# Performance work log

Measured on AMD Instinct MI355X. Metric: run time of the kernel, lower is better.

The kernel has to match this reference:

```python
import jax, jax.numpy as jnp
import numpy as np

B, CIN, COUT, H, W = 16, 64, 64, 256, 256
M1, M2 = 32, 32


def setup_inputs() -> dict:
    key = jax.random.key(0)
    k = jax.random.split(key, 7)
    x = jax.random.normal(k[0], (B, CIN, H, W), dtype=jnp.float32)
    # emulate int8 quantized weights: stored values in [-128, 127]
    q_weights1 = jax.random.randint(k[1], (CIN, COUT, M1, M2, 2), -128, 128, dtype=jnp.int32)
    q_weights2 = jax.random.randint(k[2], (CIN, COUT, M1, M2, 2), -128, 128, dtype=jnp.int32)
    w1_scale = jax.random.uniform(k[3], (1,), dtype=jnp.float32) * 0.01 + 0.001
    w1_min = jax.random.normal(k[4], (1,), dtype=jnp.float32) * 0.1
    w2_scale = jax.random.uniform(k[5], (1,), dtype=jnp.float32) * 0.01 + 0.001
    w2_min = jax.random.normal(k[6], (1,), dtype=jnp.float32) * 0.1
    return {"x": x, "q_weights1": q_weights1, "q_weights2": q_weights2,
            "w1_scale": w1_scale, "w1_min": w1_min,
            "w2_scale": w2_scale, "w2_min": w2_min}


def _dequant_complex(q, scale, min_val):
    # (q + 127) * scale + min, then view last dim (re, im) as complex
    w = (q.astype(jnp.float32) + 127.0) * scale + min_val
    return jax.lax.complex(w[..., 0], w[..., 1])


def reference(x, q_weights1, q_weights2, w1_scale, w1_min, w2_scale, w2_min):
    b, cin, h, w = x.shape
    # rfft2 with ortho norm, complex64
    x_ft = jnp.fft.rfft2(x, norm="ortho")  # [B, Cin, H, W//2+1]

    w1c = _dequant_complex(q_weights1, w1_scale[0], w1_min[0])  # [Cin, Cout, M1, M2]
    w2c = _dequant_complex(q_weights2, w2_scale[0], w2_min[0])

    # complex multiply + channel contraction on the retained low/high modes
    out1 = jnp.einsum("bixy,ioxy->boxy", x_ft[:, :, :M1, :M2], w1c)
    out2 = jnp.einsum("bixy,ioxy->boxy", x_ft[:, :, h - M1:, :M2], w2c)

    out_ft = jnp.zeros((b, COUT, h, w // 2 + 1), dtype=x_ft.dtype)
    out_ft = out_ft.at[:, :, :M1, :M2].set(out1)
    out_ft = out_ft.at[:, :, h - M1:, :M2].set(out2)

    return jnp.fft.irfft2(out_ft, s=(h, w), norm="ortho")  # [B, Cout, H, W] float32
```

## Files before the change

### kernel.cpp

```cpp
#include <hip/hip_runtime.h>
#include <math.h>

#define NB 16
#define NCIN 64
#define NCOUT 64
#define NH 256
#define NW 256
#define NM 64
#define NKX 32
#define INV256 (1.0f/256.0f)

typedef __attribute__((ext_vector_type(8))) short short8v;
typedef __attribute__((ext_vector_type(4))) float f32x4;
typedef unsigned short u16;
typedef unsigned int u32;

__device__ __forceinline__ void bf16_split(float v, u16& hi, u16& lo) {
    u32 b = __float_as_uint(v);
    u32 hib = b & 0xffff0000u;
    float lof = v - __uint_as_float(hib);
    hi = (u16)(hib >> 16);
    lo = (u16)(__float_as_uint(lof) >> 16);
}

__device__ __forceinline__ u16 bf16_rtn(float v) {
    u32 b = __float_as_uint(v);
    u32 r = b + 0x7fffu + ((b >> 16) & 1u);
    return (u16)(r >> 16);
}

__global__ __launch_bounds__(256) void init_tw(u16* __restrict__ tw) {
    const int tid = blockIdx.x * 256 + threadIdx.x;
    const float TWO_PI = 6.28318530717958647692f;
    if (tid < 16384) {
        const int e = tid & 7, lane = (tid >> 3) & 63;
        const int nt = (tid >> 9) & 3, kc = tid >> 11;
        const int w = kc * 32 + (lane >> 4) * 8 + e;
        const int n = nt * 16 + (lane & 15);
        const int kx = n >> 1, p = n & 1;
        const float ang = TWO_PI * (float)((kx * w) & 255) * INV256;
        const float v = p ? -sinf(ang) : cosf(ang);
        u16 hi, lo; bf16_split(v, hi, lo);
        tw[tid] = hi; tw[16384 + tid] = lo;
    } else {
        const int u = tid - 16384;
        const int e = u & 7, lane = (u >> 3) & 63;
        const int kc = (u >> 9) & 7, mt = u >> 12;
        const int m = mt * 16 + (lane & 15);
        const int h = kc * 32 + (lane >> 4) * 8 + e;
        const int ky = (m < 32) ? m : (192 + m);
        const float ang = TWO_PI * (float)((ky * h) & 255) * INV256;
        const float c = cosf(ang), s = sinf(ang);
        u16 hi, lo;
        bf16_split(c,  hi, lo); tw[32768 + u] = hi; tw[49152 + u]  = lo;
        bf16_split(s,  hi, lo); tw[65536 + u] = hi; tw[81920 + u]  = lo;
        bf16_split(-s, hi, lo); tw[98304 + u] = hi; tw[114688 + u] = lo;
    }
}

__global__ __launch_bounds__(256) void init_tw2(u16* __restrict__ tw2) {
    const int tid = blockIdx.x * 256 + threadIdx.x;
    const float TWO_PI = 6.28318530717958647692f;
    if (tid < 16384) {
        const int e = tid & 7, lane = (tid >> 3) & 63;
        const int kc = (tid >> 9) & 1, HT = tid >> 10;
        const int h = HT * 16 + (lane & 15);
        const int m = kc * 32 + ((lane >> 4) << 3) + e;
        const int ky = (m < 32) ? m : (192 + m);
        const float ang = TWO_PI * (float)((ky * h) & 255) * INV256;
        tw2[tid]         = bf16_rtn(cosf(ang));
        tw2[16384 + tid] = bf16_rtn(sinf(ang));
        tw2[32768 + tid] = bf16_rtn(-sinf(ang));
    } else {
        const int u = tid - 16384;
        const int e = u & 7, lane = (u >> 3) & 63;
        const int kc = (u >> 9) & 1, nt = u >> 10;
        const int w = nt * 16 + (lane & 15);
        const int kk = kc * 32 + ((lane >> 4) << 3) + e;
        const int kx = kk >> 1, c = kk & 1;
        const float wt = (kx == 0) ? 1.f : 2.f;
        const float ang = TWO_PI * (float)((kx * w) & 255) * INV256;
        const float v = c ? (-wt * sinf(ang) * INV256) : (wt * cosf(ang) * INV256);
        tw2[49152 + u] = bf16_rtn(v);
    }
}

__global__ __launch_bounds__(256) void fwd_mfma(const float* __restrict__ x,
                                                const u16* __restrict__ tw,
                                                float2* __restrict__ xft) {
    __shared__ u16 planes[4 * 32 * 264];
    const int t = threadIdx.x;
    const int lane = t & 63;
    const int wv = t >> 6;
    const int l15 = lane & 15;
    const int lk = lane >> 4;
    const float* __restrict__ xb = x + (size_t)blockIdx.x * (NH * NW);

    const u16* __restrict__ T1h = tw;
    const u16* __restrict__ T1l = tw + 16384;

    for (int mt = 0; mt < 4; ++mt) {
        const int hbase = wv * 64 + mt * 16;
        f32x4 acc[4] = {f32x4{0,0,0,0}, f32x4{0,0,0,0}, f32x4{0,0,0,0}, f32x4{0,0,0,0}};
        for (int kc = 0; kc < 8; ++kc) {
            const float* xr = xb + (size_t)(hbase + l15) * NW + kc * 32 + lk * 8;
            const float4 xa = *(const float4*)xr;
            const float4 xc = *(const float4*)(xr + 4);
            const float v[8] = {xa.x, xa.y, xa.z, xa.w, xc.x, xc.y, xc.z, xc.w};
            short8v Ah, Al;
            #pragma unroll
            for (int e = 0; e < 8; ++e) {
                u16 hi, lo; bf16_split(v[e], hi, lo);
                Ah[e] = (short)hi; Al[e] = (short)lo;
            }
            const int tbase = (kc * 4) * 512 + lane * 8;
            #pragma unroll
            for (int nt = 0; nt < 4; ++nt) {
                const short8v Bh = *(const short8v*)(T1h + tbase + nt * 512);
                const short8v Bl = *(const short8v*)(T1l + tbase + nt * 512);
                acc[nt] = __builtin_amdgcn_mfma_f32_16x16x32_bf16(Ah, Bh, acc[nt], 0, 0, 0);
                acc[nt] = __builtin_amdgcn_mfma_f32_16x16x32_bf16(Ah, Bl, acc[nt], 0, 0, 0);
                acc[nt] = __builtin_amdgcn_mfma_f32_16x16x32_bf16(Al, Bh, acc[nt], 0, 0, 0);
            }
        }
        #pragma unroll
        for (int nt = 0; nt < 4; ++nt) {
            const int n = nt * 16 + l15;
            const int kx = n >> 1, p = n & 1;
            #pragma unroll
            for (int r = 0; r < 4; ++r) {
                const int h = hbase + lk * 4 + r;
                u16 hi, lo; bf16_split(acc[nt][r], hi, lo);
                planes[(2 * p) * 8448 + kx * 264 + h] = hi;
                planes[(2 * p + 1) * 8448 + kx * 264 + h] = lo;
            }
        }
    }
    __syncthreads();

    const u16* __restrict__ C2h = tw + 32768;
    const u16* __restrict__ C2l = tw + 49152;
    const u16* __restrict__ S2h = tw + 65536;
    const u16* __restrict__ S2l = tw + 81920;
    const u16* __restrict__ Snh = tw + 98304;
    const u16* __restrict__ Snl = tw + 114688;

    f32x4 zre[2] = {f32x4{0,0,0,0}, f32x4{0,0,0,0}};
    f32x4 zim[2] = {f32x4{0,0,0,0}, f32x4{0,0,0,0}};
    for (int kc = 0; kc < 8; ++kc) {
        const int abase = (wv * 8 + kc) * 512 + lane * 8;
        const short8v Ch = *(const short8v*)(C2h + abase);
        const short8v Cl = *(const short8v*)(C2l + abase);
        const short8v Sh = *(const short8v*)(S2h + abase);
        const short8v Sl = *(const short8v*)(S2l + abase);
        const short8v Nh = *(const short8v*)(Snh + abase);
        const short8v Nl = *(const short8v*)(Snl + abase);
        #pragma unroll
        for (int nt = 0; nt < 2; ++nt) {
            const int kx = nt * 16 + l15;
            const int off = kx * 264 + kc * 32 + lk * 8;
            const short8v Yrh = *(const short8v*)(planes + off);
            const short8v Yrl = *(const short8v*)(planes + 8448 + off);
            const short8v Yih = *(const short8v*)(planes + 16896 + off);
            const short8v Yil = *(const short8v*)(planes + 25344 + off);
            zre[nt] = __builtin_amdgcn_mfma_f32_16x16x32_bf16(Ch, Yrh, zre[nt], 0, 0, 0);
            zre[nt] = __builtin_amdgcn_mfma_f32_16x16x32_bf16(Ch, Yrl, zre[nt], 0, 0, 0);
            zre[nt] = __builtin_amdgcn_mfma_f32_16x16x32_bf16(Cl, Yrh, zre[nt], 0, 0, 0);
            zre[nt] = __builtin_amdgcn_mfma_f32_16x16x32_bf16(Sh, Yih, zre[nt], 0, 0, 0);
            zre[nt] = __builtin_amdgcn_mfma_f32_16x16x32_bf16(Sh, Yil, zre[nt], 0, 0, 0);
            zre[nt] = __builtin_amdgcn_mfma_f32_16x16x32_bf16(Sl, Yih, zre[nt], 0, 0, 0);
            zim[nt] = __builtin_amdgcn_mfma_f32_16x16x32_bf16(Ch, Yih, zim[nt], 0, 0, 0);
            zim[nt] = __builtin_amdgcn_mfma_f32_16x16x32_bf16(Ch, Yil, zim[nt], 0, 0, 0);
            zim[nt] = __builtin_amdgcn_mfma_f32_16x16x32_bf16(Cl, Yih, zim[nt], 0, 0, 0);
            zim[nt] = __builtin_amdgcn_mfma_f32_16x16x32_bf16(Nh, Yrh, zim[nt], 0, 0, 0);
            zim[nt] = __builtin_amdgcn_mfma_f32_16x16x32_bf16(Nh, Yrl, zim[nt], 0, 0, 0);
            zim[nt] = __builtin_amdgcn_mfma_f32_16x16x32_bf16(Nl, Yrh, zim[nt], 0, 0, 0);
        }
    }
    float2* __restrict__ op = xft + (size_t)blockIdx.x * (NM * NKX);
    #pragma unroll
    for (int nt = 0; nt < 2; ++nt) {
        const int kx = nt * 16 + l15;
        #pragma unroll
        for (int r = 0; r < 4; ++r) {
            const int m = wv * 16 + lk * 4 + r;
            op[m * NKX + kx] = make_float2(zre[nt][r] * INV256, zim[nt][r] * INV256);
        }
    }
}

__global__ __launch_bounds__(256) void mode_v8(const float2* __restrict__ xft,
                                               const int* __restrict__ q1,
                                               const int* __restrict__ q2,
                                               const float* __restrict__ w1s,
                                               const float* __restrict__ w1m,
                                               const float* __restrict__ w2s,
                                               const float* __restrict__ w2m,
                                               float2* __restrict__ oft) {
    __shared__ float2 xs[2][8][16][8];
    __shared__ float2 ws[2][8][16][10];
    const int m  = blockIdx.x;
    const int og = blockIdx.y;
    const int kh = blockIdx.z;
    const int t = threadIdx.x;
    const int b = t >> 4, o = t & 15;
    const int mm = (m < 32) ? m : (m - 32);
    const int* __restrict__ q = (m < 32) ? q1 : q2;
    const float scale = (m < 32) ? w1s[0] : w2s[0];
    const float wmin  = (m < 32) ? w1m[0] : w2m[0];

    const int row = t >> 1;
    const int il = row >> 4, rb = row & 15, half = t & 1;

    const float4* __restrict__ xf4 = (const float4*)xft;
    const int4*   __restrict__ qi4 = (const int4*)q;
    const size_t xbase = (size_t)(rb * 64 + il) * 1024 + m * 16 + kh * 4 + half * 2;
    const size_t wbase = (size_t)(il * 64 + og * 16 + rb) * 512 + mm * 16 + kh * 4 + half * 2;

    float4 px0, px1; int4 pw0, pw1;

    #define MV8_LOAD(P)                                                        \
        px0 = xf4[xbase + (size_t)(P) * 8 * 1024];                             \
        px1 = xf4[xbase + (size_t)(P) * 8 * 1024 + 1];                         \
        pw0 = qi4[wbase + (size_t)(P) * 8 * 32768];                            \
        pw1 = qi4[wbase + (size_t)(P) * 8 * 32768 + 1];

    #define MV8_WRITE(BUF)                                                     \
        {                                                                      \
            float4* xd = (float4*)&xs[BUF][il][rb][half * 4];                  \
            xd[0] = px0; xd[1] = px1;                                          \
            float4* wd = (float4*)&ws[BUF][il][rb][half * 4];                  \
            wd[0] = make_float4(((float)pw0.x + 127.f) * scale + wmin,         \
                                ((float)pw0.y + 127.f) * scale + wmin,         \
                                ((float)pw0.z + 127.f) * scale + wmin,         \
                                ((float)pw0.w + 127.f) * scale + wmin);        \
            wd[1] = make_float4(((float)pw1.x + 127.f) * scale + wmin,         \
                                ((float)pw1.y + 127.f) * scale + wmin,         \
                                ((float)pw1.z + 127.f) * scale + wmin,         \
                                ((float)pw1.w + 127.f) * scale + wmin);        \
        }

    MV8_LOAD(0)
    MV8_WRITE(0)
    __syncthreads();

    float accr[8], acci[8];
    #pragma unroll
    for (int k = 0; k < 8; ++k) { accr[k] = 0.f; acci[k] = 0.f; }

    #pragma unroll 1
    for (int p = 0; p < 8; ++p) {
        const int cur = p & 1;
        if (p < 7) { MV8_LOAD(p + 1) }
        #pragma unroll
        for (int jl = 0; jl < 8; ++jl) {
            const float4* xr4 = (const float4*)&xs[cur][jl][b][0];
            const float4* wr4 = (const float4*)&ws[cur][jl][o][0];
            #pragma unroll
            for (int kq = 0; kq < 4; ++kq) {
                const float4 xv = xr4[kq];
                const float4 wv = wr4[kq];
                accr[2 * kq]     += xv.x * wv.x - xv.y * wv.y;
                acci[2 * kq]     += xv.x * wv.y + xv.y * wv.x;
                accr[2 * kq + 1] += xv.z * wv.z - xv.w * wv.w;
                acci[2 * kq + 1] += xv.z * wv.w + xv.w * wv.z;
            }
        }
        if (p < 7) {
            MV8_WRITE(cur ^ 1)
            __syncthreads();
        }
    }
    #undef MV8_LOAD
    #undef MV8_WRITE

    float2* __restrict__ op = oft + ((size_t)(b * 64 + og * 16 + o) * NM + m) * NKX + kh * 8;
    #pragma unroll
    for (int k = 0; k < 8; ++k) op[k] = make_float2(accr[k], acci[k]);
}

__global__ __launch_bounds__(256) void inv_mfma(const float2* __restrict__ oft,
                                                const u16* __restrict__ tw2,
                                                float* __restrict__ out) {
    __shared__ u16 lds[13824];
    const int t = threadIdx.x;
    const int lane = t & 63;
    const int wv = t >> 6;
    const int l15 = lane & 15;
    const int lk = lane >> 4;
    const int hh = blockIdx.y;

    const float2* __restrict__ ip = oft + (size_t)blockIdx.x * (NM * NKX);
    #pragma unroll
    for (int r = 0; r < 8; ++r) {
        const int idx = r * 256 + t;
        const int m = idx >> 5, kx = idx & 31;
        const float2 v = ip[idx];
        lds[kx * 72 + m]        = bf16_rtn(v.x);
        lds[2304 + kx * 72 + m] = bf16_rtn(v.y);
    }
    __syncthreads();

    const u16* __restrict__ C4 = tw2;
    const u16* __restrict__ S4 = tw2 + 16384;
    const u16* __restrict__ N4 = tw2 + 32768;

    short8v Br[2][2], Bi[2][2];
    #pragma unroll
    for (int nt = 0; nt < 2; ++nt) {
        #pragma unroll
        for (int kc = 0; kc < 2; ++kc) {
            const int off = (nt * 16 + l15) * 72 + kc * 32 + lk * 8;
            Br[nt][kc] = *(const short8v*)(lds + off);
            Bi[nt][kc] = *(const short8v*)(lds + 2304 + off);
        }
    }

    #pragma unroll
    for (int mt = 0; mt < 2; ++mt) {
        const int lt = wv * 2 + mt;
        const int HT = hh * 8 + lt;
        f32x4 zr[2] = {f32x4{0,0,0,0}, f32x4{0,0,0,0}};
        f32x4 zi[2] = {f32x4{0,0,0,0}, f32x4{0,0,0,0}};
        #pragma unroll
        for (int kc = 0; kc < 2; ++kc) {
            const int abase = ((HT * 2 + kc) * 64 + lane) * 8;
            const short8v C = *(const short8v*)(C4 + abase);
            const short8v S = *(const short8v*)(S4 + abase);
            const short8v N = *(const short8v*)(N4 + abase);
            #pragma unroll
            for (int nt = 0; nt < 2; ++nt) {
                zr[nt] = __builtin_amdgcn_mfma_f32_16x16x32_bf16(C, Br[nt][kc], zr[nt], 0, 0, 0);
                zr[nt] = __builtin_amdgcn_mfma_f32_16x16x32_bf16(N, Bi[nt][kc], zr[nt], 0, 0, 0);
                zi[nt] = __builtin_amdgcn_mfma_f32_16x16x32_bf16(S, Br[nt][kc], zi[nt], 0, 0, 0);
                zi[nt] = __builtin_amdgcn_mfma_f32_16x16x32_bf16(C, Bi[nt][kc], zi[nt], 0, 0, 0);
            }
        }
        #pragma unroll
        for (int nt = 0; nt < 2; ++nt) {
            const int kx = nt * 16 + l15;
            #pragma unroll
            for (int r = 0; r < 4; ++r) {
                const int hl = lt * 16 + lk * 4 + r;
                const u32 pk = (u32)bf16_rtn(zr[nt][r]) | ((u32)bf16_rtn(zi[nt][r]) << 16);
                *(u32*)(lds + 4608 + hl * 72 + 2 * kx) = pk;
            }
        }
    }
    __syncthreads();

    const u16* __restrict__ W5 = tw2 + 49152;
    float* __restrict__ op = out + (size_t)blockIdx.x * (NH * NW) + (size_t)hh * 128 * NW;
    for (int nt = 0; nt < 16; ++nt) {
        const short8v B0 = *(const short8v*)(W5 + ((nt * 2 + 0) * 64 + lane) * 8);
        const short8v B1 = *(const short8v*)(W5 + ((nt * 2 + 1) * 64 + lane) * 8);
        const int w = nt * 16 + l15;
        #pragma unroll
        for (int mt = 0; mt < 2; ++mt) {
            const int lt = wv * 2 + mt;
            const int h0 = lt * 16 + l15;
            const short8v A0 = *(const short8v*)(lds + 4608 + h0 * 72 + lk * 8);
            const short8v A1 = *(const short8v*)(lds + 4608 + h0 * 72 + 32 + lk * 8);
            f32x4 acc = {0, 0, 0, 0};
            acc = __builtin_amdgcn_mfma_f32_16x16x32_bf16(A0, B0, acc, 0, 0, 0);
            acc = __builtin_amdgcn_mfma_f32_16x16x32_bf16(A1, B1, acc, 0, 0, 0);
            #pragma unroll
            for (int r = 0; r < 4; ++r) {
                const int hl = lt * 16 + lk * 4 + r;
                op[hl * 256 + w] = acc[r];
            }
        }
    }
}

extern "C" void kernel_launch(void* const* d_in, const int* in_sizes, int n_in,
                              void* d_out, int out_size, void* d_ws, size_t ws_size,
                              hipStream_t stream) {
    const float* x  = (const float*)d_in[0];
    const int* q1   = (const int*)d_in[1];
    const int* q2   = (const int*)d_in[2];
    const float* w1s = (const float*)d_in[3];
    const float* w1m = (const float*)d_in[4];
    const float* w2s = (const float*)d_in[5];
    const float* w2m = (const float*)d_in[6];
    float* out = (float*)d_out;

    float2* xft = (float2*)d_ws;
    float2* oft = xft + (size_t)NB * NCIN * NM * NKX;
    u16* tw  = (u16*)((char*)d_ws + (size_t)48 * 1024 * 1024);
    u16* tw2 = tw + 131072;

    init_tw<<<128, 256, 0, stream>>>(tw);
    init_tw2<<<128, 256, 0, stream>>>(tw2);
    fwd_mfma<<<NB * NCIN, 256, 0, stream>>>(x, tw, xft);
    mode_v8<<<dim3(NM, 4, 4), 256, 0, stream>>>(xft, q1, q2, w1s, w1m, w2s, w2m, oft);
    inv_mfma<<<dim3(NB * NCOUT, 2), 256, 0, stream>>>(oft, tw2, out);
}
```

Before: 240.8 us.

## Restructure mode-mixing kernel: stage all weights once, stream x directly from global

The mode-mixing kernel is rewritten to use a finer grid (8 output-channel groups × 8 kx groups) so each block handles 8 output channels and 4 kx values. Each block dequantizes its full weight tile for all 64 input channels into LDS once, behind a single barrier. It then streams x directly from global memory with 8-deep register prefetch instead of double-buffered LDS staging with per-step barriers. This removes repeated synchronization and raises block count and parallelism. In exchange, per-thread register reuse drops (2 outputs per thread instead of 8) and x is read from global redundantly across output-channel groups.

```diff
diff --git a/kernel.cpp b/kernel.cpp
--- a/kernel.cpp
+++ b/kernel.cpp
@@ -189,94 +189,80 @@
     }
 }
 
-__global__ __launch_bounds__(256) void mode_v8(const float2* __restrict__ xft,
-                                               const int* __restrict__ q1,
-                                               const int* __restrict__ q2,
-                                               const float* __restrict__ w1s,
-                                               const float* __restrict__ w1m,
-                                               const float* __restrict__ w2s,
-                                               const float* __restrict__ w2m,
-                                               float2* __restrict__ oft) {
-    __shared__ float2 xs[2][8][16][8];
-    __shared__ float2 ws[2][8][16][10];
+__global__ __launch_bounds__(256) void mode_v10(const float2* __restrict__ xft,
+                                                const int* __restrict__ q1,
+                                                const int* __restrict__ q2,
+                                                const float* __restrict__ w1s,
+                                                const float* __restrict__ w1m,
+                                                const float* __restrict__ w2s,
+                                                const float* __restrict__ w2m,
+                                                float2* __restrict__ oft) {
+    __shared__ float wlds[4096];
     const int m  = blockIdx.x;
     const int og = blockIdx.y;
     const int kh = blockIdx.z;
     const int t = threadIdx.x;
-    const int b = t >> 4, o = t & 15;
     const int mm = (m < 32) ? m : (m - 32);
     const int* __restrict__ q = (m < 32) ? q1 : q2;
     const float scale = (m < 32) ? w1s[0] : w2s[0];
     const float wmin  = (m < 32) ? w1m[0] : w2m[0];
 
-    const int row = t >> 1;
-    const int il = row >> 4, rb = row & 15, half = t & 1;
-
+    {
+        const int4* __restrict__ qi4 = (const int4*)q;
+        int4 v[4];
+        #pragma unroll
+        for (int rr = 0; rr < 2; ++rr) {
+            const int row = t * 2 + rr;
+            const int i = row >> 3, ol = row & 7;
+            const size_t b4 = (size_t)(i * 64 + og * 8 + ol) * 512 + mm * 16 + kh * 2;
+            v[rr * 2]     = qi4[b4];
+            v[rr * 2 + 1] = qi4[b4 + 1];
+        }
+        #pragma unroll
+        for (int rr = 0; rr < 2; ++rr) {
+            const int row = t * 2 + rr;
+            float* wd = &wlds[row * 8];
+            const int4 a = v[rr * 2], bq = v[rr * 2 + 1];
+            wd[0] = ((float)a.x + 127.f) * scale + wmin;
+            wd[1] = ((float)a.y + 127.f) * scale + wmin;
+            wd[2] = ((float)a.z + 127.f) * scale + wmin;
+            wd[3] = ((float)a.w + 127.f) * scale + wmin;
+            wd[4] = ((float)bq.x + 127.f) * scale + wmin;
+            wd[5] = ((float)bq.y + 127.f) * scale + wmin;
+            wd[6] = ((float)bq.z + 127.f) * scale + wmin;
+            wd[7] = ((float)bq.w + 127.f) * scale + wmin;
+        }
+    }
+    __syncthreads();
+
+    const int b  = t >> 4;
+    const int ol = (t >> 1) & 7;
+    const int kp = t & 1;
     const float4* __restrict__ xf4 = (const float4*)xft;
-    const int4*   __restrict__ qi4 = (const int4*)q;
-    const size_t xbase = (size_t)(rb * 64 + il) * 1024 + m * 16 + kh * 4 + half * 2;
-    const size_t wbase = (size_t)(il * 64 + og * 16 + rb) * 512 + mm * 16 + kh * 4 + half * 2;
-
-    float4 px0, px1; int4 pw0, pw1;
-
-    #define MV8_LOAD(P)                                                        \
-        px0 = xf4[xbase + (size_t)(P) * 8 * 1024];                             \
-        px1 = xf4[xbase + (size_t)(P) * 8 * 1024 + 1];                         \
-        pw0 = qi4[wbase + (size_t)(P) * 8 * 32768];                            \
-        pw1 = qi4[wbase + (size_t)(P) * 8 * 32768 + 1];
-
-    #define MV8_WRITE(BUF)                                                     \
-        {                                                                      \
-            float4* xd = (float4*)&xs[BUF][il][rb][half * 4];                  \
-            xd[0] = px0; xd[1] = px1;                                          \
-            float4* wd = (float4*)&ws[BUF][il][rb][half * 4];                  \
-            wd[0] = make_float4(((float)pw0.x + 127.f) * scale + wmin,         \
-                                ((float)pw0.y + 127.f) * scale + wmin,         \
-                                ((float)pw0.z + 127.f) * scale + wmin,         \
-                                ((float)pw0.w + 127.f) * scale + wmin);        \
-            wd[1] = make_float4(((float)pw1.x + 127.f) * scale + wmin,         \
-                                ((float)pw1.y + 127.f) * scale + wmin,         \
-                                ((float)pw1.z + 127.f) * scale + wmin,         \
-                                ((float)pw1.w + 127.f) * scale + wmin);        \
-        }
-
-    MV8_LOAD(0)
-    MV8_WRITE(0)
-    __syncthreads();
-
-    float accr[8], acci[8];
-    #pragma unroll
-    for (int k = 0; k < 8; ++k) { accr[k] = 0.f; acci[k] = 0.f; }
+    const size_t xoff = (size_t)m * 16 + kh * 2 + kp;
+
+    float accr0 = 0.f, acci0 = 0.f, accr1 = 0.f, acci1 = 0.f;
 
     #pragma unroll 1
-    for (int p = 0; p < 8; ++p) {
-        const int cur = p & 1;
-        if (p < 7) { MV8_LOAD(p + 1) }
-        #pragma unroll
-        for (int jl = 0; jl < 8; ++jl) {
-            const float4* xr4 = (const float4*)&xs[cur][jl][b][0];
-            const float4* wr4 = (const float4*)&ws[cur][jl][o][0];
-            #pragma unroll
-            for (int kq = 0; kq < 4; ++kq) {
-                const float4 xv = xr4[kq];
-                const float4 wv = wr4[kq];
-                accr[2 * kq]     += xv.x * wv.x - xv.y * wv.y;
-                acci[2 * kq]     += xv.x * wv.y + xv.y * wv.x;
-                accr[2 * kq + 1] += xv.z * wv.z - xv.w * wv.w;
-                acci[2 * kq + 1] += xv.z * wv.w + xv.w * wv.z;
-            }
-        }
-        if (p < 7) {
-            MV8_WRITE(cur ^ 1)
-            __syncthreads();
-        }
-    }
-    #undef MV8_LOAD
-    #undef MV8_WRITE
-
-    float2* __restrict__ op = oft + ((size_t)(b * 64 + og * 16 + o) * NM + m) * NKX + kh * 8;
-    #pragma unroll
-    for (int k = 0; k < 8; ++k) op[k] = make_float2(accr[k], acci[k]);
+    for (int i0 = 0; i0 < 64; i0 += 8) {
+        float4 xb[8];
+        #pragma unroll
+        for (int u = 0; u < 8; ++u)
+            xb[u] = xf4[(size_t)(b * 64 + i0 + u) * 1024 + xoff];
+        #pragma unroll
+        for (int u = 0; u < 8; ++u) {
+            const float4 wv = *(const float4*)&wlds[((i0 + u) * 8 + ol) * 8 + kp * 4];
+            const float4 xv = xb[u];
+            accr0 += xv.x * wv.x - xv.y * wv.y;
+            acci0 += xv.x * wv.y + xv.y * wv.x;
+            accr1 += xv.z * wv.z - xv.w * wv.w;
+            acci1 += xv.z * wv.w + xv.w * wv.z;
+        }
+    }
+
+    float4* __restrict__ op4 = (float4*)oft;
+    op4[(size_t)((b * 64 + og * 8 + ol) * 64 + m) * 16 + kh * 2 + kp] =
+        make_float4(accr0, acci0, accr1, acci1);
 }
 
 __global__ __launch_bounds__(256) void inv_mfma(const float2* __restrict__ oft,
@@ -393,6 +379,6 @@
     init_tw<<<128, 256, 0, stream>>>(tw);
     init_tw2<<<128, 256, 0, stream>>>(tw2);
     fwd_mfma<<<NB * NCIN, 256, 0, stream>>>(x, tw, xft);
-    mode_v8<<<dim3(NM, 4, 4), 256, 0, stream>>>(xft, q1, q2, w1s, w1m, w2s, w2m, oft);
+    mode_v10<<<dim3(NM, 8, 8), 256, 0, stream>>>(xft, q1, q2, w1s, w1m, w2s, w2m, oft);
     inv_mfma<<<dim3(NB * NCOUT, 2), 256, 0, stream>>>(oft, tw2, out);
 }
```

Result: no change. 237.2 us (-1.5%).
